# Kernel optimization log

Hardware: AMD Instinct MI355X
Metric: run time of the kernel (lower is better)

The kernel has to match this reference:

```python
import jax, jax.numpy as jnp
import numpy as np

N = 20000      # num nodes
E = 320000     # num edges (avg degree 16)
F_IN = 518     # object_feature_dim
D = 128        # node_embedding_dim (= GAT out_channels)
ED = 32        # edge_embedding_dim
R = 26         # num_relations
H = 4          # GAT heads (concat=False -> mean over heads)
HID = 256      # node_encoder hidden


def _gat_layer(x, src, dst, ea, lin, lin_e, att_s, att_d, att_e, bias):
    """PyG GATConv: add_self_loops=True (fill_value='mean'), concat=False, negative_slope=0.2."""
    n = x.shape[0]
    ones = jnp.ones((src.shape[0],), x.dtype)
    cnt = jax.ops.segment_sum(ones, dst, num_segments=n)                    # [N]
    loop_ea = jax.ops.segment_sum(ea, dst, num_segments=n) / jnp.maximum(cnt, 1.0)[:, None]
    idx = jnp.arange(n)
    s = jnp.concatenate([src, idx])
    d = jnp.concatenate([dst, idx])
    ea2 = jnp.concatenate([ea, loop_ea], axis=0)                            # [E+N, ED]
    h = (x @ lin).reshape(n, H, D)                                          # [N,H,D]
    a_s = jnp.einsum('nhd,hd->nh', h, att_s)                                # [N,H]
    a_d = jnp.einsum('nhd,hd->nh', h, att_d)
    e = (ea2 @ lin_e).reshape(-1, H, D)                                     # [E+N,H,D]
    a_e = jnp.einsum('ehd,hd->eh', e, att_e)
    alpha = jax.nn.leaky_relu(a_s[s] + a_d[d] + a_e, 0.2)                   # [E+N,H]
    amax = jax.ops.segment_max(alpha, d, num_segments=n)
    alpha = jnp.exp(alpha - amax[d])
    denom = jax.ops.segment_sum(alpha, d, num_segments=n)
    alpha = alpha / (denom[d] + 1e-16)                                      # segment softmax
    msg = h[s] * alpha[:, :, None]                                          # [E+N,H,D]
    out = jax.ops.segment_sum(msg, d, num_segments=n)                       # [N,H,D]
    return out.mean(axis=1) + bias                                          # concat=False


def setup_inputs() -> dict:
    key = jax.random.key(0)
    ks = jax.random.split(key, 18)
    g = lambda k, shp, s=0.05: jax.random.normal(k, shp, jnp.float32) * s
    return {
        'x': g(ks[0], (N, F_IN), 1.0),
        'edge_index': jax.random.randint(ks[1], (2, E), 0, N),
        'edge_type': jax.random.randint(ks[2], (E,), 0, R),
        'w1': g(ks[3], (F_IN, HID)), 'b1': jnp.zeros((HID,), jnp.float32),
        'w2': g(ks[4], (HID, D)),    'b2': jnp.zeros((D,), jnp.float32),
        'rel_emb': g(ks[5], (R, ED), 1.0),
        'lin1': g(ks[6], (D, H * D)), 'line1': g(ks[7], (ED, H * D)),
        'atts1': g(ks[8], (H, D)), 'attd1': g(ks[9], (H, D)), 'atte1': g(ks[10], (H, D)),
        'bias1': jnp.zeros((D,), jnp.float32),
        'lin2': g(ks[11], (D, H * D)), 'line2': g(ks[12], (ED, H * D)),
        'atts2': g(ks[13], (H, D)), 'attd2': g(ks[14], (H, D)), 'atte2': g(ks[15], (H, D)),
        'bias2': jnp.zeros((D,), jnp.float32),
    }


def reference(x, edge_index, edge_type, w1, b1, w2, b2, rel_emb,
              lin1, line1, atts1, attd1, atte1, bias1,
              lin2, line2, atts2, attd2, atte2, bias2):
    src, dst = edge_index[0], edge_index[1]
    # node encoder (dropout inactive in eval)
    h = jax.nn.relu(x @ w1 + b1) @ w2 + b2                                  # [N,D]
    ea = rel_emb[edge_type]                                                 # [E,ED]
    h = jax.nn.relu(_gat_layer(h, src, dst, ea, lin1, line1, atts1, attd1, atte1, bias1))
    h = jax.nn.relu(_gat_layer(h, src, dst, ea, lin2, line2, atts2, attd2, atte2, bias2))
    return h
```

## Files before the change

### kernel.cpp

```cpp
#include <hip/hip_runtime.h>
#include <math.h>

#define N_NODES 20000
#define MP      20032
#define N_EDGES 320000
#define F_IN    518
#define HIDDEN  256
#define DIM     128
#define NH      4

typedef __attribute__((ext_vector_type(8))) short bf16x8;
typedef __attribute__((ext_vector_type(4))) float f32x4;
typedef unsigned short ushort_t;

__device__ __forceinline__ float lrelu02(float x) { return x > 0.f ? x : 0.2f * x; }

__device__ __forceinline__ void gl_lds16(const void* g, void* l) {
    __builtin_amdgcn_global_load_lds(
        (const __attribute__((address_space(1))) unsigned int*)g,
        (__attribute__((address_space(3))) unsigned int*)l, 16, 0, 0);
}

__device__ __forceinline__ unsigned int hi16(float v) { return __float_as_uint(v) >> 16; }
__device__ __forceinline__ unsigned int lo16(float v) {
    unsigned int h = __float_as_uint(v) & 0xFFFF0000u;
    return __float_as_uint(v - __uint_as_float(h)) >> 16;
}
__device__ __forceinline__ unsigned int rnd16(float v) {
    unsigned int u = __float_as_uint(v);
    return (u + 0x7FFFu + ((u >> 16) & 1u)) >> 16;
}
__device__ __forceinline__ float bfl(unsigned int u) { return __uint_as_float(u << 16); }
__device__ __forceinline__ float bfh(unsigned int u) { return __uint_as_float(u & 0xFFFF0000u); }

__global__ __launch_bounds__(256, 4) void gemm_mfma_v2(
    const ushort_t* __restrict__ Ah, const ushort_t* __restrict__ Al,
    const ushort_t* __restrict__ Bh, const ushort_t* __restrict__ Bl,
    const float* __restrict__ bias,
    int M, int K8, int N, int act,
    float* __restrict__ Cf,
    ushort_t* __restrict__ Ch, ushort_t* __restrict__ Cl,
    ushort_t* __restrict__ Cb,
    ushort_t* __restrict__ Ca)
{
    __shared__ __align__(16) ushort_t lds[12288];
    const int tid = threadIdx.x;
    const int w = tid >> 6, lane = tid & 63;
    const int row0 = blockIdx.y * 64, col0 = blockIdx.x * 128;
    const int nkb = K8 >> 2;
    const int m16 = lane & 15, q = lane >> 4;
    const bool use_al = (Al != nullptr);

    f32x4 acc[4][2] = {};

    for (int kb = 0; kb < nkb; ++kb) {
        const size_t kc = (size_t)(kb * 4 + w);
        const size_t aoff = (kc * MP + row0) * 8 + lane * 8;
        const size_t boff = (kc * N + col0) * 8 + lane * 8;
        gl_lds16(Ah + aoff, &lds[w * 512]);
        if (use_al) gl_lds16(Al + aoff, &lds[2048 + w * 512]);
        gl_lds16(Bh + boff,       &lds[4096 + w * 1024]);
        gl_lds16(Bh + boff + 512, &lds[4096 + w * 1024 + 512]);
        gl_lds16(Bl + boff,       &lds[8192 + w * 1024]);
        gl_lds16(Bl + boff + 512, &lds[8192 + w * 1024 + 512]);
        __syncthreads();

        bf16x8 fah[4], fal[4], fbh[2], fbl[2];
        const int fa = q * 512 + m16 * 8;
        #pragma unroll
        for (int mi = 0; mi < 4; ++mi) {
            fah[mi] = *(const bf16x8*)&lds[fa + mi * 128];
            if (use_al) fal[mi] = *(const bf16x8*)&lds[2048 + fa + mi * 128];
        }
        const int fb = q * 1024 + (w * 32 + m16) * 8;
        #pragma unroll
        for (int ni = 0; ni < 2; ++ni) {
            fbh[ni] = *(const bf16x8*)&lds[4096 + fb + ni * 128];
            fbl[ni] = *(const bf16x8*)&lds[8192 + fb + ni * 128];
        }
        #pragma unroll
        for (int mi = 0; mi < 4; ++mi)
            #pragma unroll
            for (int ni = 0; ni < 2; ++ni) {
                acc[mi][ni] = __builtin_amdgcn_mfma_f32_16x16x32_bf16(fah[mi], fbh[ni], acc[mi][ni], 0, 0, 0);
                acc[mi][ni] = __builtin_amdgcn_mfma_f32_16x16x32_bf16(fah[mi], fbl[ni], acc[mi][ni], 0, 0, 0);
            }
        if (use_al) {
            #pragma unroll
            for (int mi = 0; mi < 4; ++mi)
                #pragma unroll
                for (int ni = 0; ni < 2; ++ni)
                    acc[mi][ni] = __builtin_amdgcn_mfma_f32_16x16x32_bf16(fal[mi], fbh[ni], acc[mi][ni], 0, 0, 0);
        }
        __syncthreads();
    }

    #pragma unroll
    for (int ni = 0; ni < 2; ++ni) {
        const int col = col0 + w * 32 + ni * 16 + m16;
        const float bb = bias ? bias[col] : 0.f;
        #pragma unroll
        for (int mi = 0; mi < 4; ++mi) {
            #pragma unroll
            for (int r = 0; r < 4; ++r) {
                const int row = row0 + mi * 16 + q * 4 + r;
                if (row < M) {
                    float v = acc[mi][ni][r] + bb;
                    if (act) v = fmaxf(v, 0.f);
                    if (Cf) Cf[(size_t)row * N + col] = v;
                    if (Cb) Cb[(size_t)row * N + col] = (ushort_t)rnd16(v);
                    const size_t p = (((size_t)(col >> 3)) * MP + row) * 8 + (col & 7);
                    if (Ch) { Ch[p] = (ushort_t)hi16(v); Cl[p] = (ushort_t)lo16(v); }
                    if (Ca) Ca[p] = (ushort_t)rnd16(v);
                }
            }
        }
    }
}

__global__ __launch_bounds__(256) void conv_a_t_kernel(
    const float* __restrict__ x, ushort_t* __restrict__ xh, ushort_t* __restrict__ xl)
{
    __shared__ float tile[64][68];
    const int tid = threadIdx.x;
    const int r0 = blockIdx.x * 64;
    const int c0 = blockIdx.y * 64;

    #pragma unroll
    for (int it = 0; it < 4; ++it) {
        const int r = (tid >> 4) + it * 16;
        const int c = (tid & 15) * 4;
        const int gr = r0 + r, gc = c0 + c;
        float4 v = {0.f, 0.f, 0.f, 0.f};
        if (gr < N_NODES) {
            if (gc + 3 < F_IN) {
                v = *(const float4*)(x + (size_t)gr * F_IN + gc);
            } else {
                float tmp[4] = {0.f, 0.f, 0.f, 0.f};
                #pragma unroll
                for (int u = 0; u < 4; ++u)
                    if (gc + u < F_IN) tmp[u] = x[(size_t)gr * F_IN + gc + u];
                v.x = tmp[0]; v.y = tmp[1]; v.z = tmp[2]; v.w = tmp[3];
            }
        }
        tile[r][c] = v.x; tile[r][c+1] = v.y; tile[r][c+2] = v.z; tile[r][c+3] = v.w;
    }
    __syncthreads();

    const int k8l = tid >> 5;
    const int k8 = (c0 >> 3) + k8l;
    if (k8 >= 68) return;
    const int rr = (tid & 31) * 2;
    #pragma unroll
    for (int u = 0; u < 2; ++u) {
        const int r = rr + u;
        unsigned int hp[4], lp[4];
        #pragma unroll
        for (int i = 0; i < 4; ++i) {
            const float v0 = tile[r][k8l * 8 + 2 * i];
            const float v1 = tile[r][k8l * 8 + 2 * i + 1];
            hp[i] = (hi16(v1) << 16) | hi16(v0);
            lp[i] = (lo16(v1) << 16) | lo16(v0);
        }
        const size_t p = ((size_t)k8 * MP + r0 + r) * 8;
        *(uint4*)(xh + p) = make_uint4(hp[0], hp[1], hp[2], hp[3]);
        *(uint4*)(xl + p) = make_uint4(lp[0], lp[1], lp[2], lp[3]);
    }
}

__global__ __launch_bounds__(256) void conv_b_kernel(
    const float* __restrict__ w, ushort_t* __restrict__ bh, ushort_t* __restrict__ bl,
    int K, int N, int total)
{
    const int idx = blockIdx.x * 256 + threadIdx.x;
    if (idx >= total) return;
    const int j = idx & 7;
    const int rem = idx >> 3;
    const int n = rem % N;
    const int k = (rem / N) * 8 + j;
    const float v = (k < K) ? w[(size_t)k * N + n] : 0.f;
    bh[idx] = (ushort_t)hi16(v);
    bl[idx] = (ushort_t)lo16(v);
}

__global__ __launch_bounds__(256) void wa_kernel(
    const float* __restrict__ lin, const float* __restrict__ atts,
    const float* __restrict__ attd, float* __restrict__ wa_s, float* __restrict__ wa_d)
{
    const int wrk = blockIdx.x * 256 + threadIdx.x;
    if (wrk >= 1024) return;
    const int sd = wrk >> 9;
    const int p = wrk & 511;
    const int h = p >> 7, d = p & 127;
    const float* av = (sd ? attd : atts) + h * DIM;
    const float* lp = lin + (size_t)d * (NH * DIM) + h * DIM;
    float acc = 0.f;
    #pragma unroll 8
    for (int i = 0; i < DIM; ++i) acc += lp[i] * av[i];
    (sd ? wa_d : wa_s)[h * DIM + d] = acc;
}

__global__ __launch_bounds__(256) void as_ad_kernel(
    const float* __restrict__ xb, const float* __restrict__ wa_s,
    const float* __restrict__ wa_d, float* __restrict__ a_s, float* __restrict__ a_d)
{
    const int gw = blockIdx.x * 4 + (threadIdx.x >> 6);
    const int lane = threadIdx.x & 63;
    if (gw >= N_NODES * NH) return;
    const int n = gw >> 2, h = gw & 3;
    const float* hp = xb + (size_t)n * DIM;
    float2 hv = *(const float2*)(hp + lane * 2);
    float2 sv = *(const float2*)(wa_s + h * DIM + lane * 2);
    float2 dv = *(const float2*)(wa_d + h * DIM + lane * 2);
    float s = hv.x * sv.x + hv.y * sv.y;
    float d = hv.x * dv.x + hv.y * dv.y;
    #pragma unroll
    for (int off = 32; off > 0; off >>= 1) {
        s += __shfl_down(s, off);
        d += __shfl_down(d, off);
    }
    if (lane == 0) { a_s[n * 4 + h] = s; a_d[n * 4 + h] = d; }
}

__global__ __launch_bounds__(128) void rel_table_kernel(
    const float* __restrict__ rel_emb, const float* __restrict__ line,
    const float* __restrict__ atte, float* __restrict__ table)
{
    __shared__ float we[32][NH];
    const int tid = threadIdx.x;
    const int k = tid >> 2, h = tid & 3;
    float acc = 0.f;
    for (int d = 0; d < DIM; ++d)
        acc += line[(size_t)k * (NH * DIM) + h * DIM + d] * atte[h * DIM + d];
    we[k][h] = acc;
    __syncthreads();
    if (tid < 26 * NH) {
        int r = tid >> 2, hh = tid & 3;
        float t = 0.f;
        for (int kk = 0; kk < 32; ++kk) t += rel_emb[r * 32 + kk] * we[kk][hh];
        table[r * 4 + hh] = t;
    }
}

__global__ __launch_bounds__(256) void hist_kernel(
    const int* __restrict__ dst, int* __restrict__ cnt)
{
    const int e = blockIdx.x * blockDim.x + threadIdx.x;
    if (e >= N_EDGES) return;
    atomicAdd(&cnt[dst[e]], 1);
}

__global__ __launch_bounds__(1024) void scan_kernel(
    const int* __restrict__ cnt, int* __restrict__ ptr, int* __restrict__ ptr_copy)
{
    __shared__ int tsum[1024];
    const int tid = threadIdx.x;
    const int CH = 20;
    const int base = tid * CH;
    int s = 0;
    #pragma unroll
    for (int i = 0; i < CH; ++i) {
        int idx = base + i;
        if (idx < N_NODES) s += cnt[idx];
    }
    tsum[tid] = s;
    __syncthreads();
    for (int off = 1; off < 1024; off <<= 1) {
        int v = (tid >= off) ? tsum[tid - off] : 0;
        __syncthreads();
        tsum[tid] += v;
        __syncthreads();
    }
    int run = (tid == 0) ? 0 : tsum[tid - 1];
    #pragma unroll
    for (int i = 0; i < CH; ++i) {
        int idx = base + i;
        if (idx < N_NODES) {
            ptr[idx] = run;
            ptr_copy[idx] = run;
            run += cnt[idx];
        }
    }
    if (tid == 0) ptr[N_NODES] = N_EDGES;
}

__global__ __launch_bounds__(256) void scatter_kernel(
    const int* __restrict__ src, const int* __restrict__ dst, const int* __restrict__ etype,
    int* __restrict__ ptr_copy, int2* __restrict__ se)
{
    const int e = blockIdx.x * blockDim.x + threadIdx.x;
    if (e >= N_EDGES) return;
    const int d = dst[e];
    const int pos = atomicAdd(&ptr_copy[d], 1);
    se[pos] = make_int2(src[e], etype[e]);
}

__global__ __launch_bounds__(256) void node_agg_kernel(
    const int* __restrict__ ptr, const int2* __restrict__ se,
    const float* __restrict__ a_s, const float* __restrict__ a_d,
    const float* __restrict__ table, const ushort_t* __restrict__ hb,
    const float* __restrict__ bias,
    float* __restrict__ outf, ushort_t* __restrict__ oa)
{
    const int n = blockIdx.x * 4 + (threadIdx.x >> 6);
    const int lane = threadIdx.x & 63;
    if (n >= N_NODES) return;
    const int beg = ptr[n], end = ptr[n + 1];
    const int head = lane >> 4;
    const int cbase = lane * 8;
    const float adh = a_d[n * 4 + head];

    float acc[8] = {};
    float dh = 0.f, eh = 0.f;

    int j = beg;
    for (; j + 2 <= end; j += 2) {
        const int2 E0 = se[j], E1 = se[j + 1];
        const uint4 g0 = *(const uint4*)(hb + (size_t)E0.x * 512 + cbase);
        const uint4 g1 = *(const uint4*)(hb + (size_t)E1.x * 512 + cbase);
        const float a0 = a_s[E0.x * 4 + head];
        const float t0 = table[E0.y * 4 + head];
        const float a1 = a_s[E1.x * 4 + head];
        const float t1 = table[E1.y * 4 + head];
        const float p0 = __expf(lrelu02(a0 + adh + t0));
        const float p1 = __expf(lrelu02(a1 + adh + t1));
        eh += t0 + t1;
        dh += p0 + p1;
        acc[0] += p0 * bfl(g0.x) + p1 * bfl(g1.x);
        acc[1] += p0 * bfh(g0.x) + p1 * bfh(g1.x);
        acc[2] += p0 * bfl(g0.y) + p1 * bfl(g1.y);
        acc[3] += p0 * bfh(g0.y) + p1 * bfh(g1.y);
        acc[4] += p0 * bfl(g0.z) + p1 * bfl(g1.z);
        acc[5] += p0 * bfh(g0.z) + p1 * bfh(g1.z);
        acc[6] += p0 * bfl(g0.w) + p1 * bfl(g1.w);
        acc[7] += p0 * bfh(g0.w) + p1 * bfh(g1.w);
    }
    if (j < end) {
        const int2 E0 = se[j];
        const uint4 g0 = *(const uint4*)(hb + (size_t)E0.x * 512 + cbase);
        const float a0 = a_s[E0.x * 4 + head];
        const float t0 = table[E0.y * 4 + head];
        const float p0 = __expf(lrelu02(a0 + adh + t0));
        eh += t0;
        dh += p0;
        acc[0] += p0 * bfl(g0.x); acc[1] += p0 * bfh(g0.x);
        acc[2] += p0 * bfl(g0.y); acc[3] += p0 * bfh(g0.y);
        acc[4] += p0 * bfl(g0.z); acc[5] += p0 * bfh(g0.z);
        acc[6] += p0 * bfl(g0.w); acc[7] += p0 * bfh(g0.w);
    }

    const float inv = 1.0f / fmaxf((float)(end - beg), 1.0f);
    const float ps = __expf(lrelu02(a_s[n * 4 + head] + adh + eh * inv));
    dh += ps;
    {
        const uint4 gs = *(const uint4*)(hb + (size_t)n * 512 + cbase);
        acc[0] += ps * bfl(gs.x); acc[1] += ps * bfh(gs.x);
        acc[2] += ps * bfl(gs.y); acc[3] += ps * bfh(gs.y);
        acc[4] += ps * bfl(gs.z); acc[5] += ps * bfh(gs.z);
        acc[6] += ps * bfl(gs.w); acc[7] += ps * bfh(gs.w);
    }

    const float ih = 0.25f / (dh + 1e-16f);
    float t[8];
    #pragma unroll
    for (int k = 0; k < 8; ++k) {
        t[k] = acc[k] * ih;
        t[k] += __shfl_xor(t[k], 16);
        t[k] += __shfl_xor(t[k], 32);
    }
    if (lane < 16) {
        const float4 b0 = *(const float4*)(bias + cbase);
        const float4 b1 = *(const float4*)(bias + cbase + 4);
        float o[8];
        o[0] = fmaxf(t[0] + b0.x, 0.f); o[1] = fmaxf(t[1] + b0.y, 0.f);
        o[2] = fmaxf(t[2] + b0.z, 0.f); o[3] = fmaxf(t[3] + b0.w, 0.f);
        o[4] = fmaxf(t[4] + b1.x, 0.f); o[5] = fmaxf(t[5] + b1.y, 0.f);
        o[6] = fmaxf(t[6] + b1.z, 0.f); o[7] = fmaxf(t[7] + b1.w, 0.f);
        if (outf) {
            float4 v0 = {o[0], o[1], o[2], o[3]};
            float4 v1 = {o[4], o[5], o[6], o[7]};
            *(float4*)(outf + (size_t)n * DIM + cbase) = v0;
            *(float4*)(outf + (size_t)n * DIM + cbase + 4) = v1;
        }
        if (oa) {
            unsigned int up[4];
            #pragma unroll
            for (int i = 0; i < 4; ++i)
                up[i] = (rnd16(o[2*i+1]) << 16) | rnd16(o[2*i]);
            *(uint4*)(oa + ((size_t)lane * MP + n) * 8) = make_uint4(up[0], up[1], up[2], up[3]);
        }
    }
}

extern "C" void kernel_launch(void* const* d_in, const int* in_sizes, int n_in,
                              void* d_out, int out_size, void* d_ws, size_t ws_size,
                              hipStream_t stream)
{
    const float* x       = (const float*)d_in[0];
    const int*   eidx    = (const int*)d_in[1];
    const int*   etype   = (const int*)d_in[2];
    const float* w1      = (const float*)d_in[3];
    const float* b1      = (const float*)d_in[4];
    const float* w2      = (const float*)d_in[5];
    const float* b2      = (const float*)d_in[6];
    const float* rel_emb = (const float*)d_in[7];
    const float* lin[2]  = {(const float*)d_in[8],  (const float*)d_in[14]};
    const float* line[2] = {(const float*)d_in[9],  (const float*)d_in[15]};
    const float* atts[2] = {(const float*)d_in[10], (const float*)d_in[16]};
    const float* attd[2] = {(const float*)d_in[11], (const float*)d_in[17]};
    const float* atte[2] = {(const float*)d_in[12], (const float*)d_in[18]};
    const float* bias[2] = {(const float*)d_in[13], (const float*)d_in[19]};
    const int* src = eidx;
    const int* dst = eidx + N_EDGES;

    char* base = (char*)d_ws;
    size_t off = 0;
    auto alloc = [&](size_t bytes) -> void* {
        void* p = base + off;
        off = (off + bytes + 255) & ~(size_t)255;
        return p;
    };
    ushort_t* xh  = (ushort_t*)alloc((size_t)68 * MP * 8 * 2);
    ushort_t* xl  = (ushort_t*)alloc((size_t)68 * MP * 8 * 2);
    ushort_t* h1h = (ushort_t*)alloc((size_t)32 * MP * 8 * 2);
    ushort_t* h1l = (ushort_t*)alloc((size_t)32 * MP * 8 * 2);
    ushort_t* x0a = (ushort_t*)alloc((size_t)16 * MP * 8 * 2);
    void* reg1    = alloc((size_t)16 * MP * 8 * 4);
    ushort_t* w1h = (ushort_t*)alloc(68 * 256 * 8 * 2);
    ushort_t* w1l = (ushort_t*)alloc(68 * 256 * 8 * 2);
    ushort_t* w2h = (ushort_t*)alloc(32 * 128 * 8 * 2);
    ushort_t* w2l = (ushort_t*)alloc(32 * 128 * 8 * 2);
    ushort_t* l0h = (ushort_t*)alloc(16 * 512 * 8 * 2);
    ushort_t* l0l = (ushort_t*)alloc(16 * 512 * 8 * 2);
    ushort_t* l1h = (ushort_t*)alloc(16 * 512 * 8 * 2);
    ushort_t* l1l = (ushort_t*)alloc(16 * 512 * 8 * 2);
    float* a_s   = (float*)alloc(N_NODES * 4 * 4);
    float* a_d   = (float*)alloc(N_NODES * 4 * 4);
    float* table = (float*)alloc(128 * 4);
    float* wa_s  = (float*)alloc(512 * 4);
    float* wa_d  = (float*)alloc(512 * 4);
    int*  cnt_i  = (int*)alloc(N_NODES * 4);
    int*  ptr    = (int*)alloc((N_NODES + 4) * 4);
    int*  ptrc   = (int*)alloc(N_NODES * 4);
    int2* se     = (int2*)alloc((size_t)N_EDGES * 8);

    ushort_t* hb = xh;
    float* xbuf1 = (float*)h1h;
    float* xbuf0 = (float*)reg1;
    ushort_t* x1a = (ushort_t*)reg1;

    const int mtiles = MP / 64;

    conv_a_t_kernel<<<dim3(MP / 64, 9), 256, 0, stream>>>(x, xh, xl);
    conv_b_kernel<<<(68*256*8 + 255) / 256, 256, 0, stream>>>(w1, w1h, w1l, F_IN, HIDDEN, 68*256*8);
    conv_b_kernel<<<(32*128*8 + 255) / 256, 256, 0, stream>>>(w2, w2h, w2l, HIDDEN, DIM, 32*128*8);
    conv_b_kernel<<<(16*512*8 + 255) / 256, 256, 0, stream>>>(lin[0], l0h, l0l, DIM, NH*DIM, 16*512*8);
    conv_b_kernel<<<(16*512*8 + 255) / 256, 256, 0, stream>>>(lin[1], l1h, l1l, DIM, NH*DIM, 16*512*8);

    hipMemsetAsync(cnt_i, 0, N_NODES * sizeof(int), stream);
    hist_kernel<<<(N_EDGES + 255) / 256, 256, 0, stream>>>(dst, cnt_i);
    scan_kernel<<<1, 1024, 0, stream>>>(cnt_i, ptr, ptrc);
    scatter_kernel<<<(N_EDGES + 255) / 256, 256, 0, stream>>>(src, dst, etype, ptrc, se);

    gemm_mfma_v2<<<dim3(HIDDEN / 128, mtiles), 256, 0, stream>>>(
        xh, xl, w1h, w1l, b1, N_NODES, 68, HIDDEN, 1, nullptr, h1h, h1l, nullptr, nullptr);
    gemm_mfma_v2<<<dim3(DIM / 128, mtiles), 256, 0, stream>>>(
        h1h, h1l, w2h, w2l, b2, N_NODES, 32, DIM, 0, xbuf0, nullptr, nullptr, nullptr, x0a);

    gemm_mfma_v2<<<dim3((NH * DIM) / 128, mtiles), 256, 0, stream>>>(
        x0a, nullptr, l0h, l0l, nullptr, N_NODES, 16, NH * DIM, 0, nullptr, nullptr, nullptr, hb, nullptr);
    wa_kernel<<<4, 256, 0, stream>>>(lin[0], atts[0], attd[0], wa_s, wa_d);
    as_ad_kernel<<<N_NODES, 256, 0, stream>>>(xbuf0, wa_s, wa_d, a_s, a_d);
    rel_table_kernel<<<1, 128, 0, stream>>>(rel_emb, line[0], atte[0], table);
    node_agg_kernel<<<(N_NODES + 3) / 4, 256, 0, stream>>>(
        ptr, se, a_s, a_d, table, hb, bias[0], xbuf1, x1a);

    gemm_mfma_v2<<<dim3((NH * DIM) / 128, mtiles), 256, 0, stream>>>(
        x1a, nullptr, l1h, l1l, nullptr, N_NODES, 16, NH * DIM, 0, nullptr, nullptr, nullptr, hb, nullptr);
    wa_kernel<<<4, 256, 0, stream>>>(lin[1], atts[1], attd[1], wa_s, wa_d);
    as_ad_kernel<<<N_NODES, 256, 0, stream>>>(xbuf1, wa_s, wa_d, a_s, a_d);
    rel_table_kernel<<<1, 128, 0, stream>>>(rel_emb, line[1], atte[1], table);
    node_agg_kernel<<<(N_NODES + 3) / 4, 256, 0, stream>>>(
        ptr, se, a_s, a_d, table, hb, bias[1], (float*)d_out, nullptr);
}
```

Measured before the change: 444.4 us.

## Fuse layer-2 attention scores into layer-1 aggregation and unroll edge loop by four

Folds the per-node a_s/a_d projection for the second GAT layer into the epilogue of the first aggregation kernel, using shuffle reductions across the 16 lanes of each head. This removes one as_ad_kernel launch, the fp32 xbuf1 write and its re-read. The edge loop is also unrolled to four edges so more gathers are in flight at once, at the cost of extra registers. The wa weight preparation moves earlier and now uses separate buffers for each layer.

```diff
diff --git a/kernel.cpp b/kernel.cpp
--- a/kernel.cpp
+++ b/kernel.cpp
@@ -300,7 +300,9 @@
     const float* __restrict__ a_s, const float* __restrict__ a_d,
     const float* __restrict__ table, const ushort_t* __restrict__ hb,
     const float* __restrict__ bias,
-    float* __restrict__ outf, ushort_t* __restrict__ oa)
+    float* __restrict__ outf, ushort_t* __restrict__ oa,
+    const float* __restrict__ wa_s2, const float* __restrict__ wa_d2,
+    float* __restrict__ a_s2, float* __restrict__ a_d2)
 {
     const int n = blockIdx.x * 4 + (threadIdx.x >> 6);
     const int lane = threadIdx.x & 63;
@@ -314,35 +316,34 @@
     float dh = 0.f, eh = 0.f;
 
     int j = beg;
-    for (; j + 2 <= end; j += 2) {
-        const int2 E0 = se[j], E1 = se[j + 1];
-        const uint4 g0 = *(const uint4*)(hb + (size_t)E0.x * 512 + cbase);
-        const uint4 g1 = *(const uint4*)(hb + (size_t)E1.x * 512 + cbase);
-        const float a0 = a_s[E0.x * 4 + head];
-        const float t0 = table[E0.y * 4 + head];
-        const float a1 = a_s[E1.x * 4 + head];
-        const float t1 = table[E1.y * 4 + head];
-        const float p0 = __expf(lrelu02(a0 + adh + t0));
-        const float p1 = __expf(lrelu02(a1 + adh + t1));
-        eh += t0 + t1;
-        dh += p0 + p1;
-        acc[0] += p0 * bfl(g0.x) + p1 * bfl(g1.x);
-        acc[1] += p0 * bfh(g0.x) + p1 * bfh(g1.x);
-        acc[2] += p0 * bfl(g0.y) + p1 * bfl(g1.y);
-        acc[3] += p0 * bfh(g0.y) + p1 * bfh(g1.y);
-        acc[4] += p0 * bfl(g0.z) + p1 * bfl(g1.z);
-        acc[5] += p0 * bfh(g0.z) + p1 * bfh(g1.z);
-        acc[6] += p0 * bfl(g0.w) + p1 * bfl(g1.w);
-        acc[7] += p0 * bfh(g0.w) + p1 * bfh(g1.w);
-    }
-    if (j < end) {
+    for (; j + 4 <= end; j += 4) {
+        int2 E[4];
+        E[0] = se[j]; E[1] = se[j + 1]; E[2] = se[j + 2]; E[3] = se[j + 3];
+        uint4 g[4];
+        float av[4], tv[4];
+        #pragma unroll
+        for (int u = 0; u < 4; ++u) {
+            g[u] = *(const uint4*)(hb + (size_t)E[u].x * 512 + cbase);
+            av[u] = a_s[E[u].x * 4 + head];
+            tv[u] = table[E[u].y * 4 + head];
+        }
+        #pragma unroll
+        for (int u = 0; u < 4; ++u) {
+            const float p = __expf(lrelu02(av[u] + adh + tv[u]));
+            eh += tv[u]; dh += p;
+            acc[0] += p * bfl(g[u].x); acc[1] += p * bfh(g[u].x);
+            acc[2] += p * bfl(g[u].y); acc[3] += p * bfh(g[u].y);
+            acc[4] += p * bfl(g[u].z); acc[5] += p * bfh(g[u].z);
+            acc[6] += p * bfl(g[u].w); acc[7] += p * bfh(g[u].w);
+        }
+    }
+    for (; j < end; ++j) {
         const int2 E0 = se[j];
         const uint4 g0 = *(const uint4*)(hb + (size_t)E0.x * 512 + cbase);
         const float a0 = a_s[E0.x * 4 + head];
         const float t0 = table[E0.y * 4 + head];
         const float p0 = __expf(lrelu02(a0 + adh + t0));
-        eh += t0;
-        dh += p0;
+        eh += t0; dh += p0;
         acc[0] += p0 * bfl(g0.x); acc[1] += p0 * bfh(g0.x);
         acc[2] += p0 * bfl(g0.y); acc[3] += p0 * bfh(g0.y);
         acc[4] += p0 * bfl(g0.z); acc[5] += p0 * bfh(g0.z);
@@ -388,6 +389,33 @@
             for (int i = 0; i < 4; ++i)
                 up[i] = (rnd16(o[2*i+1]) << 16) | rnd16(o[2*i]);
             *(uint4*)(oa + ((size_t)lane * MP + n) * 8) = make_uint4(up[0], up[1], up[2], up[3]);
+        }
+        if (wa_s2) {
+            float pss[4] = {0,0,0,0}, pdd[4] = {0,0,0,0};
+            #pragma unroll
+            for (int h = 0; h < NH; ++h) {
+                const float* ws = wa_s2 + h * DIM + cbase;
+                const float* wd = wa_d2 + h * DIM + cbase;
+                #pragma unroll
+                for (int i = 0; i < 8; ++i) {
+                    pss[h] += o[i] * ws[i];
+                    pdd[h] += o[i] * wd[i];
+                }
+            }
+            #pragma unroll
+            for (int m = 1; m < 16; m <<= 1) {
+                #pragma unroll
+                for (int h = 0; h < NH; ++h) {
+                    pss[h] += __shfl_xor(pss[h], m);
+                    pdd[h] += __shfl_xor(pdd[h], m);
+                }
+            }
+            if (lane == 0) {
+                float4 vs = {pss[0], pss[1], pss[2], pss[3]};
+                float4 vd = {pdd[0], pdd[1], pdd[2], pdd[3]};
+                *(float4*)(a_s2 + n * 4) = vs;
+                *(float4*)(a_d2 + n * 4) = vd;
+            }
         }
     }
 }
@@ -434,18 +462,21 @@
     ushort_t* l0l = (ushort_t*)alloc(16 * 512 * 8 * 2);
     ushort_t* l1h = (ushort_t*)alloc(16 * 512 * 8 * 2);
     ushort_t* l1l = (ushort_t*)alloc(16 * 512 * 8 * 2);
-    float* a_s   = (float*)alloc(N_NODES * 4 * 4);
-    float* a_d   = (float*)alloc(N_NODES * 4 * 4);
+    float* a_s0  = (float*)alloc(N_NODES * 4 * 4);
+    float* a_d0  = (float*)alloc(N_NODES * 4 * 4);
+    float* a_s1  = (float*)alloc(N_NODES * 4 * 4);
+    float* a_d1  = (float*)alloc(N_NODES * 4 * 4);
     float* table = (float*)alloc(128 * 4);
-    float* wa_s  = (float*)alloc(512 * 4);
-    float* wa_d  = (float*)alloc(512 * 4);
+    float* wa_s0 = (float*)alloc(512 * 4);
+    float* wa_d0 = (float*)alloc(512 * 4);
+    float* wa_s1 = (float*)alloc(512 * 4);
+    float* wa_d1 = (float*)alloc(512 * 4);
     int*  cnt_i  = (int*)alloc(N_NODES * 4);
     int*  ptr    = (int*)alloc((N_NODES + 4) * 4);
     int*  ptrc   = (int*)alloc(N_NODES * 4);
     int2* se     = (int2*)alloc((size_t)N_EDGES * 8);
 
     ushort_t* hb = xh;
-    float* xbuf1 = (float*)h1h;
     float* xbuf0 = (float*)reg1;
     ushort_t* x1a = (ushort_t*)reg1;
 
@@ -456,6 +487,8 @@
     conv_b_kernel<<<(32*128*8 + 255) / 256, 256, 0, stream>>>(w2, w2h, w2l, HIDDEN, DIM, 32*128*8);
     conv_b_kernel<<<(16*512*8 + 255) / 256, 256, 0, stream>>>(lin[0], l0h, l0l, DIM, NH*DIM, 16*512*8);
     conv_b_kernel<<<(16*512*8 + 255) / 256, 256, 0, stream>>>(lin[1], l1h, l1l, DIM, NH*DIM, 16*512*8);
+    wa_kernel<<<4, 256, 0, stream>>>(lin[0], atts[0], attd[0], wa_s0, wa_d0);
+    wa_kernel<<<4, 256, 0, stream>>>(lin[1], atts[1], attd[1], wa_s1, wa_d1);
 
     hipMemsetAsync(cnt_i, 0, N_NODES * sizeof(int), stream);
     hist_kernel<<<(N_EDGES + 255) / 256, 256, 0, stream>>>(dst, cnt_i);
@@ -469,17 +502,16 @@
 
     gemm_mfma_v2<<<dim3((NH * DIM) / 128, mtiles), 256, 0, stream>>>(
         x0a, nullptr, l0h, l0l, nullptr, N_NODES, 16, NH * DIM, 0, nullptr, nullptr, nullptr, hb, nullptr);
-    wa_kernel<<<4, 256, 0, stream>>>(lin[0], atts[0], attd[0], wa_s, wa_d);
-    as_ad_kernel<<<N_NODES, 256, 0, stream>>>(xbuf0, wa_s, wa_d, a_s, a_d);
+    as_ad_kernel<<<N_NODES, 256, 0, stream>>>(xbuf0, wa_s0, wa_d0, a_s0, a_d0);
     rel_table_kernel<<<1, 128, 0, stream>>>(rel_emb, line[0], atte[0], table);
     node_agg_kernel<<<(N_NODES + 3) / 4, 256, 0, stream>>>(
-        ptr, se, a_s, a_d, table, hb, bias[0], xbuf1, x1a);
+        ptr, se, a_s0, a_d0, table, hb, bias[0], nullptr, x1a,
+        wa_s1, wa_d1, a_s1, a_d1);
 
     gemm_mfma_v2<<<dim3((NH * DIM) / 128, mtiles), 256, 0, stream>>>(
         x1a, nullptr, l1h, l1l, nullptr, N_NODES, 16, NH * DIM, 0, nullptr, nullptr, nullptr, hb, nullptr);
-    wa_kernel<<<4, 256, 0, stream>>>(lin[1], atts[1], attd[1], wa_s, wa_d);
-    as_ad_kernel<<<N_NODES, 256, 0, stream>>>(xbuf1, wa_s, wa_d, a_s, a_d);
     rel_table_kernel<<<1, 128, 0, stream>>>(rel_emb, line[1], atte[1], table);
     node_agg_kernel<<<(N_NODES + 3) / 4, 256, 0, stream>>>(
-        ptr, se, a_s, a_d, table, hb, bias[1], (float*)d_out, nullptr);
-}
+        ptr, se, a_s1, a_d1, table, hb, bias[1], (float*)d_out, nullptr,
+        nullptr, nullptr, nullptr, nullptr);
+}
```

Result: no change. 440.2 us (-0.9%).
